# Optimization experiments

Measured on AMD Instinct MI355X. Metric: run time of the kernel, lower is better.

Reference implementation:

```python
import jax, jax.numpy as jnp
import numpy as np

A, D, F = 2048, 64, 12  # atoms, depth, filter_length


def _chemconv(x, conn, bond, filters):
    # x: (A, D); conn: (A, A, F); bond: (A, F, 2); filters: (D, F, D+2)
    # node_connection = conn.transpose(1,2) @ x -> (A, F, D)
    ncon = jnp.einsum('anf,nd->afd', conn, x)
    combined = jnp.concatenate([ncon, bond], axis=2)  # (A, F, D+2)
    # broadcast-multiply by filters then sum over last two dims -> (A, out_depth)
    return jnp.einsum('afc,ofc->ao', combined, filters)


def setup_inputs() -> dict:
    key = jax.random.key(0)
    k1, k2, k3, k4, k5 = jax.random.split(key, 5)
    x = jax.random.normal(k1, (A, D), dtype=jnp.float32)
    conn = jax.random.uniform(k2, (A, A, F), dtype=jnp.float32)
    bond = jax.random.normal(k3, (A, F, 2), dtype=jnp.float32)
    scale = 1.0 / D  # filters.data.normal_() * (1/in_depth)
    f0 = jax.random.normal(k4, (D, F, D + 2), dtype=jnp.float32) * scale
    f1 = jax.random.normal(k5, (D, F, D + 2), dtype=jnp.float32) * scale
    return {
        'node_property_tensor': x,
        'connectivity_tensor': conn,
        'bond_property_tensor': bond,
        'filters0': f0,
        'filters1': f1,
    }


def reference(node_property_tensor, connectivity_tensor, bond_property_tensor, filters0, filters1):
    x = node_property_tensor
    out = x
    for filt in (filters0, filters1):
        # each ChemConv layer is applied twice (same weights), per the torch code
        out = jax.nn.relu(_chemconv(out, connectivity_tensor, bond_property_tensor, filt))
        out = _chemconv(out, connectivity_tensor, bond_property_tensor, filt)
        out = out + x  # residual to the original block input
        out = jax.nn.relu(out)
    return out
```

## Files before the change

### kernel.cpp

```cpp
#include <hip/hip_runtime.h>


#define A_N 2048
#define D_N 64
#define F_N 12
#define K_TOTAL (A_N * F_N)
#define NSPLIT 48
#define KSEG (K_TOTAL / NSPLIT)
#define BK 64
#define NKB (KSEG / BK)

typedef short short8 __attribute__((ext_vector_type(8)));
typedef float f32x16 __attribute__((ext_vector_type(16)));

#define GLOAD16(ldsp, gp)                                                        \
  __builtin_amdgcn_global_load_lds(                                              \
      (const __attribute__((address_space(1))) void*)(gp),                       \
      (__attribute__((address_space(3))) void*)(ldsp), 16, 0, 0)

__device__ __forceinline__ unsigned pk_bf16(float a, float b) {
  unsigned ua = __float_as_uint(a);
  unsigned ub = __float_as_uint(b);
  ua += 0x7fffu + ((ua >> 16) & 1u);
  ub += 0x7fffu + ((ub >> 16) & 1u);
  return (ua >> 16) | (ub & 0xffff0000u);
}

__device__ __forceinline__ unsigned short bf16_1(float v) {
  unsigned u = __float_as_uint(v);
  u += 0x7fffu + ((u >> 16) & 1u);
  return (unsigned short)(u >> 16);
}

__global__ void k_conv(const float* __restrict__ conn, unsigned short* __restrict__ connt) {
  int atile = blockIdx.x, ks = blockIdx.y;
  int t = threadIdx.x, lane = t & 63, w = t >> 6;
  unsigned short* tile = connt + (size_t)(atile * 48 + ks) * 65536;
  int kb = lane >> 3, j = lane & 7;
#pragma unroll 4
  for (int p = 0; p < 32; ++p) {
    int row = w * 32 + p;
    const float4* src = (const float4*)(conn + (size_t)(atile * 128 + row) * K_TOTAL +
                                        ks * 512 + lane * 8);
    float4 a = src[0];
    float4 b = src[1];
    uint4 o;
    o.x = pk_bf16(a.x, a.y);
    o.y = pk_bf16(a.z, a.w);
    o.z = pk_bf16(b.x, b.y);
    o.w = pk_bf16(b.z, b.w);
    *(uint4*)(tile + ((kb * 128 + row) * 8 + j) * 8) = o;
  }
}

__global__ void k_transpose_x(const float* __restrict__ x, float* __restrict__ xt) {
  __shared__ float ld[64][65];
  int m0 = blockIdx.x * 64;
  int t = threadIdx.x;
  int r = t >> 2, cq = (t & 3) * 16;
  const float4* src = (const float4*)(x + (size_t)(m0 + r) * 64 + cq);
#pragma unroll
  for (int i = 0; i < 4; ++i) {
    float4 v = src[i];
    ld[r][cq + i * 4 + 0] = v.x;
    ld[r][cq + i * 4 + 1] = v.y;
    ld[r][cq + i * 4 + 2] = v.z;
    ld[r][cq + i * 4 + 3] = v.w;
  }
  __syncthreads();
  int c = t >> 2, ml0 = (t & 3) * 16;
  float4* dst = (float4*)(xt + (size_t)c * 2048 + m0 + ml0);
#pragma unroll
  for (int i = 0; i < 4; ++i) {
    float4 v;
    v.x = ld[ml0 + i * 4 + 0][c];
    v.y = ld[ml0 + i * 4 + 1][c];
    v.z = ld[ml0 + i * 4 + 2][c];
    v.w = ld[ml0 + i * 4 + 3][c];
    dst[i] = v;
  }
}

__global__ void k_bterm(const float* __restrict__ bond, const float* __restrict__ f0,
                        const float* __restrict__ f1, float* __restrict__ bt0,
                        float* __restrict__ bt1) {
  int a = blockIdx.x * 64 + (threadIdx.x & 63);
  int o = blockIdx.y * 4 + (threadIdx.x >> 6);
  float s0 = 0.f, s1 = 0.f;
#pragma unroll
  for (int f = 0; f < F_N; ++f) {
#pragma unroll
    for (int j = 0; j < 2; ++j) {
      float bv = bond[a * 24 + f * 2 + j];
      s0 += bv * f0[o * 792 + f * 66 + 64 + j];
      s1 += bv * f1[o * 792 + f * 66 + 64 + j];
    }
  }
  bt0[o * 2048 + a] = s0;
  bt1[o * 2048 + a] = s1;
}

__global__ void k_g(const float* __restrict__ vt, const float* __restrict__ filt,
                    unsigned short* __restrict__ gtt) {
  __shared__ float W[12][64];
  int o = blockIdx.y;
  int t = threadIdx.x;
  for (int i = t; i < 768; i += 256) W[i >> 6][i & 63] = filt[o * 792 + (i >> 6) * 66 + (i & 63)];
  __syncthreads();
  int n = blockIdx.x * 256 + t;
  float acc[12] = {0.f, 0.f, 0.f, 0.f, 0.f, 0.f, 0.f, 0.f, 0.f, 0.f, 0.f, 0.f};
#pragma unroll 4
  for (int d = 0; d < 64; ++d) {
    float v = vt[d * 2048 + n];
#pragma unroll
    for (int f = 0; f < F_N; ++f) acc[f] += v * W[f][d];
  }
  int kbase = n * 12;
#pragma unroll
  for (int f = 0; f < F_N; ++f) {
    int k = kbase + f;
    int ks = k >> 9, kb = (k >> 6) & 7, c = k & 63;
    gtt[(((size_t)ks * 8 + kb) * 64 + o) * 64 + c] = bf16_1(acc[f]);
  }
}

__launch_bounds__(256, 3)
__global__ void k_big(const unsigned short* __restrict__ connt,
                      const unsigned short* __restrict__ gtt, float* __restrict__ part) {
  __shared__ __align__(16) unsigned short smem[24576];
  int t = threadIdx.x, lane = t & 63, w = t >> 6;
  int atile = blockIdx.x, ks = blockIdx.y;
  const unsigned short* ct = connt + (size_t)(atile * 48 + ks) * 65536;
  const unsigned short* gs = gtt + (size_t)ks * 32768;

  int rl = lane >> 3, sl = lane & 7;
  int cs = sl ^ rl;

  int cSrc[4], gSrc[2];
  unsigned short *cDst[4], *gDst[2];
#pragma unroll
  for (int j = 0; j < 4; ++j) {
    cSrc[j] = (w * 32 + j * 8 + rl) * 64 + cs * 8;
    cDst[j] = smem + (w * 32 + j * 8) * 64;
  }
#pragma unroll
  for (int j = 0; j < 2; ++j) {
    gSrc[j] = (w * 16 + j * 8 + rl) * 64 + cs * 8;
    gDst[j] = smem + 16384 + (w * 16 + j * 8) * 64;
  }

  f32x16 acc0, acc1;
#pragma unroll
  for (int i = 0; i < 16; ++i) { acc0[i] = 0.f; acc1[i] = 0.f; }

  int oh = w >> 1, ah = w & 1;
  int orow = oh * 32 + (lane & 31);
  int arow = ah * 64 + (lane & 31);
  int sw = lane & 7;
  int khalf = lane >> 5;

#pragma unroll
  for (int j = 0; j < 4; ++j) GLOAD16(cDst[j], ct + cSrc[j]);
#pragma unroll
  for (int j = 0; j < 2; ++j) GLOAD16(gDst[j], gs + gSrc[j]);

  for (int kb = 0; kb < NKB; ++kb) {
    __syncthreads();
    if (kb + 1 < NKB) {
      int b = (kb + 1) & 1;
      int co = (kb + 1) * 8192, go = (kb + 1) * 4096;
#pragma unroll
      for (int j = 0; j < 4; ++j) GLOAD16(cDst[j] + b * 8192, ct + co + cSrc[j]);
#pragma unroll
      for (int j = 0; j < 2; ++j) GLOAD16(gDst[j] + b * 4096, gs + go + gSrc[j]);
    }
    const unsigned short* cb = smem + (kb & 1) * 8192;
    const unsigned short* gb = smem + 16384 + (kb & 1) * 4096;
#pragma unroll
    for (int kk = 0; kk < 4; ++kk) {
      int c = kk * 2 + khalf;
      int coff = ((c ^ sw) << 3);
      short8 af = *(const short8*)(gb + orow * 64 + coff);
      short8 b0 = *(const short8*)(cb + arow * 64 + coff);
      short8 b1 = *(const short8*)(cb + (arow + 32) * 64 + coff);
      acc0 = __builtin_amdgcn_mfma_f32_32x32x16_bf16(af, b0, acc0, 0, 0, 0);
      acc1 = __builtin_amdgcn_mfma_f32_32x32x16_bf16(af, b1, acc1, 0, 0, 0);
    }
  }

  float* pp = part + (size_t)ks * (64 * 2048);
  int a0 = atile * 128 + ah * 64 + (lane & 31);
  int ob = oh * 32 + 4 * khalf;
#pragma unroll
  for (int rg = 0; rg < 16; ++rg) {
    int o = ob + (rg & 3) + 8 * (rg >> 2);
    pp[o * 2048 + a0] = acc0[rg];
    pp[o * 2048 + a0 + 32] = acc1[rg];
  }
}

__global__ void k_reduce(const float* __restrict__ part, const float* __restrict__ bt,
                         const float* __restrict__ xt, float* __restrict__ curt,
                         float* __restrict__ outp, int residual, int final_layer) {
  int idx = blockIdx.x * 256 + threadIdx.x;
  float s = bt[idx];
#pragma unroll
  for (int sI = 0; sI < NSPLIT; ++sI) s += part[(size_t)sI * (64 * 2048) + idx];
  if (residual) s += xt[idx];
  s = fmaxf(s, 0.f);
  curt[idx] = s;
  if (final_layer) {
    int o = idx >> 11, m = idx & 2047;
    outp[m * 64 + o] = s;
  }
}

extern "C" void kernel_launch(void* const* d_in, const int* in_sizes, int n_in,
                              void* d_out, int out_size, void* d_ws, size_t ws_size,
                              hipStream_t stream) {
  const float* x    = (const float*)d_in[0];
  const float* conn = (const float*)d_in[1];
  const float* bond = (const float*)d_in[2];
  const float* f0   = (const float*)d_in[3];
  const float* f1   = (const float*)d_in[4];
  float* out = (float*)d_out;

  char* ws = (char*)d_ws;
  float* xt   = (float*)(ws + 0);
  float* curt = (float*)(ws + 524288);
  float* bt0  = (float*)(ws + 1048576);
  float* bt1  = (float*)(ws + 1572864);
  unsigned short* gtt = (unsigned short*)(ws + 2097152);
  float* part = (float*)(ws + 5242880);
  unsigned short* connt = (unsigned short*)(ws + 33554432);

  k_conv<<<dim3(16, 48), 256, 0, stream>>>(conn, connt);
  k_transpose_x<<<32, 256, 0, stream>>>(x, xt);
  k_bterm<<<dim3(32, 16), 256, 0, stream>>>(bond, f0, f1, bt0, bt1);

  for (int layer = 0; layer < 4; ++layer) {
    const float* filt = (layer < 2) ? f0 : f1;
    const float* bt   = (layer < 2) ? bt0 : bt1;
    const float* vin  = (layer == 0) ? xt : curt;
    k_g<<<dim3(8, 64), 256, 0, stream>>>(vin, filt, gtt);
    k_big<<<dim3(16, NSPLIT), 256, 0, stream>>>(connt, gtt, part);
    k_reduce<<<512, 256, 0, stream>>>(part, bt, xt, curt, out, layer & 1, layer == 3);
  }
}
```

Baseline: 496.5 us.

## Fuse fp32-to-bf16 connectivity conversion into first-layer GEMM and merge prep kernels

The separate conversion kernel that read the fp32 connectivity tensor and wrote a bf16 tiled copy is removed. The first layer's GEMM now loads fp32 conn into registers, converts to bf16, writes it to LDS for its own MFMA use, and also stores the tiled copy for later layers. This saves one full read and write pass plus a launch. The x-transpose and bond-term kernels are merged into one launch. The trade-off is that the first GEMM now prefetches through registers instead of async global-to-LDS loads, which adds register pressure and may expose latency.

```diff
diff --git a/kernel.cpp b/kernel.cpp
--- a/kernel.cpp
+++ b/kernel.cpp
@@ -32,72 +32,53 @@
   return (unsigned short)(u >> 16);
 }
 
-__global__ void k_conv(const float* __restrict__ conn, unsigned short* __restrict__ connt) {
-  int atile = blockIdx.x, ks = blockIdx.y;
-  int t = threadIdx.x, lane = t & 63, w = t >> 6;
-  unsigned short* tile = connt + (size_t)(atile * 48 + ks) * 65536;
-  int kb = lane >> 3, j = lane & 7;
-#pragma unroll 4
-  for (int p = 0; p < 32; ++p) {
-    int row = w * 32 + p;
-    const float4* src = (const float4*)(conn + (size_t)(atile * 128 + row) * K_TOTAL +
-                                        ks * 512 + lane * 8);
-    float4 a = src[0];
-    float4 b = src[1];
-    uint4 o;
-    o.x = pk_bf16(a.x, a.y);
-    o.y = pk_bf16(a.z, a.w);
-    o.z = pk_bf16(b.x, b.y);
-    o.w = pk_bf16(b.z, b.w);
-    *(uint4*)(tile + ((kb * 128 + row) * 8 + j) * 8) = o;
-  }
-}
-
-__global__ void k_transpose_x(const float* __restrict__ x, float* __restrict__ xt) {
-  __shared__ float ld[64][65];
-  int m0 = blockIdx.x * 64;
+__global__ void k_prep(const float* __restrict__ x, float* __restrict__ xt,
+                       const float* __restrict__ bond, const float* __restrict__ f0,
+                       const float* __restrict__ f1, float* __restrict__ bt0,
+                       float* __restrict__ bt1) {
   int t = threadIdx.x;
-  int r = t >> 2, cq = (t & 3) * 16;
-  const float4* src = (const float4*)(x + (size_t)(m0 + r) * 64 + cq);
-#pragma unroll
-  for (int i = 0; i < 4; ++i) {
-    float4 v = src[i];
-    ld[r][cq + i * 4 + 0] = v.x;
-    ld[r][cq + i * 4 + 1] = v.y;
-    ld[r][cq + i * 4 + 2] = v.z;
-    ld[r][cq + i * 4 + 3] = v.w;
-  }
-  __syncthreads();
-  int c = t >> 2, ml0 = (t & 3) * 16;
-  float4* dst = (float4*)(xt + (size_t)c * 2048 + m0 + ml0);
-#pragma unroll
-  for (int i = 0; i < 4; ++i) {
-    float4 v;
-    v.x = ld[ml0 + i * 4 + 0][c];
-    v.y = ld[ml0 + i * 4 + 1][c];
-    v.z = ld[ml0 + i * 4 + 2][c];
-    v.w = ld[ml0 + i * 4 + 3][c];
-    dst[i] = v;
-  }
-}
-
-__global__ void k_bterm(const float* __restrict__ bond, const float* __restrict__ f0,
-                        const float* __restrict__ f1, float* __restrict__ bt0,
-                        float* __restrict__ bt1) {
-  int a = blockIdx.x * 64 + (threadIdx.x & 63);
-  int o = blockIdx.y * 4 + (threadIdx.x >> 6);
-  float s0 = 0.f, s1 = 0.f;
-#pragma unroll
-  for (int f = 0; f < F_N; ++f) {
-#pragma unroll
-    for (int j = 0; j < 2; ++j) {
-      float bv = bond[a * 24 + f * 2 + j];
-      s0 += bv * f0[o * 792 + f * 66 + 64 + j];
-      s1 += bv * f1[o * 792 + f * 66 + 64 + j];
-    }
-  }
-  bt0[o * 2048 + a] = s0;
-  bt1[o * 2048 + a] = s1;
+  if (blockIdx.x < 32) {
+    __shared__ float ld[64][65];
+    int m0 = blockIdx.x * 64;
+    int r = t >> 2, cq = (t & 3) * 16;
+    const float4* src = (const float4*)(x + (size_t)(m0 + r) * 64 + cq);
+#pragma unroll
+    for (int i = 0; i < 4; ++i) {
+      float4 v = src[i];
+      ld[r][cq + i * 4 + 0] = v.x;
+      ld[r][cq + i * 4 + 1] = v.y;
+      ld[r][cq + i * 4 + 2] = v.z;
+      ld[r][cq + i * 4 + 3] = v.w;
+    }
+    __syncthreads();
+    int c = t >> 2, ml0 = (t & 3) * 16;
+    float4* dst = (float4*)(xt + (size_t)c * 2048 + m0 + ml0);
+#pragma unroll
+    for (int i = 0; i < 4; ++i) {
+      float4 v;
+      v.x = ld[ml0 + i * 4 + 0][c];
+      v.y = ld[ml0 + i * 4 + 1][c];
+      v.z = ld[ml0 + i * 4 + 2][c];
+      v.w = ld[ml0 + i * 4 + 3][c];
+      dst[i] = v;
+    }
+  } else {
+    int b = blockIdx.x - 32;
+    int a = (b & 31) * 64 + (t & 63);
+    int o = (b >> 5) * 4 + (t >> 6);
+    float s0 = 0.f, s1 = 0.f;
+#pragma unroll
+    for (int f = 0; f < F_N; ++f) {
+#pragma unroll
+      for (int j = 0; j < 2; ++j) {
+        float bv = bond[a * 24 + f * 2 + j];
+        s0 += bv * f0[o * 792 + f * 66 + 64 + j];
+        s1 += bv * f1[o * 792 + f * 66 + 64 + j];
+      }
+    }
+    bt0[o * 2048 + a] = s0;
+    bt1[o * 2048 + a] = s1;
+  }
 }
 
 __global__ void k_g(const float* __restrict__ vt, const float* __restrict__ filt,
@@ -125,6 +106,96 @@
 }
 
 __launch_bounds__(256, 3)
+__global__ void k_big1(const float* __restrict__ conn, const unsigned short* __restrict__ gtt,
+                       unsigned short* __restrict__ connt, float* __restrict__ part) {
+  __shared__ __align__(16) unsigned short smem[24576];
+  int t = threadIdx.x, lane = t & 63, w = t >> 6;
+  int atile = blockIdx.x, ks = blockIdx.y;
+  const float* cs0 = conn + (size_t)atile * 128 * K_TOTAL + ks * 512;
+  unsigned short* tile = connt + (size_t)(atile * 48 + ks) * 65536;
+  const unsigned short* gs = gtt + (size_t)ks * 32768;
+
+  int q0 = w * 64 + lane;
+  int gOff[8], lOff[8];
+#pragma unroll
+  for (int s = 0; s < 8; ++s) {
+    int q = q0 + s * 256;
+    int row = q >> 4, c16 = q & 15, c = c16 >> 1;
+    gOff[s] = row * K_TOTAL + c16 * 4;
+    lOff[s] = row * 64 + ((c ^ (row & 7)) << 3) + ((c16 & 1) << 2);
+  }
+
+  int rl = lane >> 3, sl = lane & 7;
+  int csz = sl ^ rl;
+  int gSrc[2];
+  unsigned short* gDst[2];
+#pragma unroll
+  for (int j = 0; j < 2; ++j) {
+    gSrc[j] = (w * 16 + j * 8 + rl) * 64 + csz * 8;
+    gDst[j] = smem + 16384 + (w * 16 + j * 8) * 64;
+  }
+
+  f32x16 acc0, acc1;
+#pragma unroll
+  for (int i = 0; i < 16; ++i) { acc0[i] = 0.f; acc1[i] = 0.f; }
+
+  int oh = w >> 1, ah = w & 1;
+  int orow = oh * 32 + (lane & 31);
+  int arow = ah * 64 + (lane & 31);
+  int sw = lane & 7;
+  int khalf = lane >> 5;
+
+  float4 rg[8];
+#pragma unroll
+  for (int s = 0; s < 8; ++s) rg[s] = *(const float4*)(cs0 + gOff[s]);
+  GLOAD16(gDst[0], gs + gSrc[0]);
+  GLOAD16(gDst[1], gs + gSrc[1]);
+
+  for (int kb = 0; kb < NKB; ++kb) {
+    unsigned short* cb = smem + (kb & 1) * 8192;
+    uint2* tb = (uint2*)tile + kb * 2048;
+#pragma unroll
+    for (int s = 0; s < 8; ++s) {
+      uint2 p;
+      p.x = pk_bf16(rg[s].x, rg[s].y);
+      p.y = pk_bf16(rg[s].z, rg[s].w);
+      *(uint2*)(cb + lOff[s]) = p;
+      tb[q0 + s * 256] = p;
+    }
+    __syncthreads();
+    if (kb + 1 < NKB) {
+      int b = (kb + 1) & 1;
+      GLOAD16(gDst[0] + b * 4096, gs + (kb + 1) * 4096 + gSrc[0]);
+      GLOAD16(gDst[1] + b * 4096, gs + (kb + 1) * 4096 + gSrc[1]);
+      const float* nsrc = cs0 + (kb + 1) * 64;
+#pragma unroll
+      for (int s = 0; s < 8; ++s) rg[s] = *(const float4*)(nsrc + gOff[s]);
+    }
+    const unsigned short* gb = smem + 16384 + (kb & 1) * 4096;
+#pragma unroll
+    for (int kk = 0; kk < 4; ++kk) {
+      int c = kk * 2 + khalf;
+      int coff = ((c ^ sw) << 3);
+      short8 af = *(const short8*)(gb + orow * 64 + coff);
+      short8 b0 = *(const short8*)(cb + arow * 64 + coff);
+      short8 b1 = *(const short8*)(cb + (arow + 32) * 64 + coff);
+      acc0 = __builtin_amdgcn_mfma_f32_32x32x16_bf16(af, b0, acc0, 0, 0, 0);
+      acc1 = __builtin_amdgcn_mfma_f32_32x32x16_bf16(af, b1, acc1, 0, 0, 0);
+    }
+  }
+
+  float* pp = part + (size_t)ks * (64 * 2048);
+  int a0 = atile * 128 + ah * 64 + (lane & 31);
+  int ob = oh * 32 + 4 * khalf;
+#pragma unroll
+  for (int rg2 = 0; rg2 < 16; ++rg2) {
+    int o = ob + (rg2 & 3) + 8 * (rg2 >> 2);
+    pp[o * 2048 + a0] = acc0[rg2];
+    pp[o * 2048 + a0 + 32] = acc1[rg2];
+  }
+}
+
+__launch_bounds__(256, 3)
 __global__ void k_big(const unsigned short* __restrict__ connt,
                       const unsigned short* __restrict__ gtt, float* __restrict__ part) {
   __shared__ __align__(16) unsigned short smem[24576];
@@ -234,16 +305,17 @@
   float* part = (float*)(ws + 5242880);
   unsigned short* connt = (unsigned short*)(ws + 33554432);
 
-  k_conv<<<dim3(16, 48), 256, 0, stream>>>(conn, connt);
-  k_transpose_x<<<32, 256, 0, stream>>>(x, xt);
-  k_bterm<<<dim3(32, 16), 256, 0, stream>>>(bond, f0, f1, bt0, bt1);
+  k_prep<<<544, 256, 0, stream>>>(x, xt, bond, f0, f1, bt0, bt1);
 
   for (int layer = 0; layer < 4; ++layer) {
     const float* filt = (layer < 2) ? f0 : f1;
     const float* bt   = (layer < 2) ? bt0 : bt1;
     const float* vin  = (layer == 0) ? xt : curt;
     k_g<<<dim3(8, 64), 256, 0, stream>>>(vin, filt, gtt);
-    k_big<<<dim3(16, NSPLIT), 256, 0, stream>>>(connt, gtt, part);
+    if (layer == 0)
+      k_big1<<<dim3(16, NSPLIT), 256, 0, stream>>>(conn, gtt, connt, part);
+    else
+      k_big<<<dim3(16, NSPLIT), 256, 0, stream>>>(connt, gtt, part);
     k_reduce<<<512, 256, 0, stream>>>(part, bt, xt, curt, out, layer & 1, layer == 3);
   }
 }
```

New measurement: 474.8 us. 1.05x faster.
